# Optimization experiments

Hardware: AMD Instinct MI355X
Metric: run time of the kernel (lower is better)

## Reference

```python
import jax, jax.numpy as jnp
from jax import lax
import numpy as np

SIGMA = 0.4        # guided-attention diagonal width
PAD_MAG = 1e12     # -inf surrogate used by the torch viterbi


def _viterbi_align(logp, text_lens, mel_lens):
    """Monotonic forced alignment. logp: (B, L, T). Returns hard alignment (B, L, T)."""
    B, L, T = logp.shape
    neg = jnp.asarray(-PAD_MAG, logp.dtype)
    # ---- forward DP over time (lax.scan replaces the python loop over T) ----
    init = jnp.full((B, L), neg, logp.dtype).at[:, 0].set(logp[:, 0, 0])
    lp_T = jnp.moveaxis(logp, 2, 0)  # (T, B, L)

    def fwd(prev, lp_t):
        # transition: stay at same text token, or advance by one (shift down along L)
        shifted = jnp.concatenate([jnp.full((B, 1), neg, logp.dtype), prev[:, :-1]], axis=1)
        cur = jnp.maximum(prev, shifted) + lp_t
        return cur, cur

    _, betas = lax.scan(fwd, init, lp_T[1:])
    log_beta = jnp.concatenate([init[None], betas], axis=0)  # (T, B, L), indexed [t, b, l]

    # ---- backtracking (faithful to the float row/col arithmetic in the source) ----
    barange = jnp.arange(B)
    rows0 = (text_lens - 1).astype(logp.dtype)
    cols0 = (mel_lens - 1).astype(logp.dtype)

    def bwd(carry, _):
        rows, cols = carry
        r = rows.astype(jnp.int32)
        c = cols.astype(jnp.int32)
        cm1 = (c - 1) % T  # torch negative indexing wraps; emulate with mod
        g_go = log_beta[cm1, barange, (r - 1) % L]
        g_stay = log_beta[cm1, barange, r % L]
        is_go = (g_go > g_stay).astype(logp.dtype)
        new_rows = jnp.maximum(rows - is_go + 1.0, 0.0) - 1.0  # relu(x)-1 as in source
        new_cols = jnp.maximum(cols, 0.0) - 1.0
        return (new_rows, new_cols), new_rows

    _, rows_seq = lax.scan(bwd, (rows0, cols0), None, length=T - 1)  # r_1 .. r_{T-1}
    path = jnp.concatenate([rows_seq[::-1], rows0[None]], axis=0).T  # (B, T)

    # one-hot over text positions (static width L instead of path.max()+1)
    align = (path[:, :, None] == jnp.arange(L, dtype=path.dtype)[None, None, :]).astype(logp.dtype)  # (B,T,L)

    # per-batch shift: drop first (T - mel_len) frames, zero-pad at the end
    pad = T - mel_lens  # (B,)
    t_idx = jnp.arange(T)[None, :] + pad[:, None]  # (B, T)
    valid = (t_idx < T)
    gathered = jnp.take_along_axis(align, jnp.clip(t_idx, 0, T - 1)[:, :, None], axis=1)
    align = gathered * valid[:, :, None].astype(logp.dtype)
    return jnp.swapaxes(align, 1, 2)  # (B, L, T)


def _guided_attention_loss(att_ws, ilens, olens, sigma=SIGMA):
    """att_ws: (B, T_out, T_in). Masked guided-attention loss (scalar)."""
    B, T, L = att_ws.shape
    t = jnp.arange(T, dtype=att_ws.dtype)[None, :, None]
    l = jnp.arange(L, dtype=att_ws.dtype)[None, None, :]
    il = ilens.astype(att_ws.dtype)[:, None, None]
    ol = olens.astype(att_ws.dtype)[:, None, None]
    w = 1.0 - jnp.exp(-((l / il - t / ol) ** 2) / (2.0 * sigma * sigma))
    valid = (t < ol) & (l < il)
    return jnp.sum(jnp.where(valid, w * att_ws, 0.0)) / jnp.sum(olens).astype(att_ws.dtype)


def setup_inputs() -> dict:
    key = jax.random.key(0)
    k1, k2, k3, k4 = jax.random.split(key, 4)
    B, L, T = 32, 256, 2048
    log_prob_matrix = jax.nn.log_softmax(jax.random.normal(k1, (B, L, T), jnp.float32), axis=1)
    att_ws = jax.nn.softmax(jax.random.normal(k2, (B, T, L), jnp.float32), axis=-1)
    text_lengths = jax.random.randint(k3, (B,), L // 2, L + 1, dtype=jnp.int32)
    mel_lengths = jax.random.randint(k4, (B,), T // 2, T + 1, dtype=jnp.int32)
    return {
        "log_prob_matrix": log_prob_matrix,
        "att_ws": att_ws,
        "text_lengths": text_lengths,
        "mel_lengths": mel_lengths,
    }


def reference(log_prob_matrix, att_ws, text_lengths, mel_lengths):
    # n_frames_per_step = 1 -> olens = mel_lengths (clamped to att width T, trivially true)
    loss = _guided_attention_loss(att_ws, text_lengths, mel_lengths)
    align = _viterbi_align(log_prob_matrix, text_lengths, mel_lengths)
    return loss, align
```

## Files before the change

### kernel.cpp

```cpp
#include <hip/hip_runtime.h>
#include <cstdint>

#define NEG (-1e12f)
constexpr int Bn = 32, Ln = 256, Tn = 2048;
constexpr int TB = Tn / 64;


__device__ inline float dpp_ror1(float x) {
    int xi = __float_as_int(x);
    return __int_as_float(__builtin_amdgcn_update_dpp(xi, xi, 0x13C, 0xF, 0xF, false));
}

__device__ inline uint32_t lds_off(const void* p) {
    return (uint32_t)(uintptr_t)(__attribute__((address_space(3))) const void*)p;
}

#define BARRIER() { asm volatile("" ::: "memory"); \
                    __builtin_amdgcn_s_barrier(); \
                    asm volatile("" ::: "memory"); }

#define DSRX(DST, ROW, BUF) \
    asm volatile("ds_read_b128 %0, %1 offset:%c2" \
        : "=&v"(DST) \
        : "v"((((ROW) >> 2) & 1) ? vxb : vxa), \
          "i"((BUF) * 16384 + ((ROW) & 15) * 1024));

#define W4 { asm volatile("s_waitcnt lgkmcnt(4)"); __builtin_amdgcn_sched_barrier(0); }

#define ABIT(ACC, X, Y) \
    asm("v_cmp_gt_f32 vcc, %1, %2\n\tv_addc_co_u32 %0, vcc, %0, %0, vcc" \
        : "+v"(ACC) : "v"(X), "v"(Y) : "vcc");

#define STEPS(S, Q) { \
    if ((((S) - 1) & 32) == 0) { ABIT(a0hi, svp, pv0) } else { ABIT(a0lo, svp, pv0) } \
    float c3 = fmaxf(pv3, pv2) + (Q).w; \
    float sv = dpp_ror1(c3); \
    float c2 = fmaxf(pv2, pv1) + (Q).z; \
    float c1 = fmaxf(pv1, pv0) + (Q).y; \
    float lf = isl0 ? negc : svp; \
    float c0 = fmaxf(pv0, lf) + (Q).x; \
    if (((S) & 32) == 0) { \
        ABIT(a1hi, c0, c1) ABIT(a2hi, c1, c2) ABIT(a3hi, c2, c3) \
    } else { \
        ABIT(a1lo, c0, c1) ABIT(a2lo, c1, c2) ABIT(a3lo, c2, c3) \
    } \
    if ((S) == 63) { \
        bb[(size_t)(4 * lane + 1) * TB + m] = ((uint64_t)a1hi << 32) | a1lo; \
        bb[(size_t)(4 * lane + 2) * TB + m] = ((uint64_t)a2hi << 32) | a2lo; \
        bb[(size_t)(4 * lane + 3) * TB + m] = ((uint64_t)a3hi << 32) | a3lo; \
        a1lo = a1hi = a2lo = a2hi = a3lo = a3hi = 0; \
    } \
    if ((S) == 64) { \
        bb[(size_t)(4 * lane + 0) * TB + m] = ((uint64_t)a0hi << 32) | a0lo; \
        a0lo = a0hi = 0; \
    } \
    pv0 = c0; pv1 = c1; pv2 = c2; pv3 = c3; svp = sv; }

#define COMP16X(I) { \
    W4 \
    STEPS(16*(I)+ 1, qq0) STEPS(16*(I)+ 2, qq1) STEPS(16*(I)+ 3, qq2) STEPS(16*(I)+ 4, qq3) \
    DSRX(qq0,  9, (I)) DSRX(qq1, 10, (I)) DSRX(qq2, 11, (I)) DSRX(qq3, 12, (I)) \
    W4 \
    STEPS(16*(I)+ 5, qq4) STEPS(16*(I)+ 6, qq5) STEPS(16*(I)+ 7, qq6) STEPS(16*(I)+ 8, qq7) \
    DSRX(qq4, 13, (I)) DSRX(qq5, 14, (I)) DSRX(qq6, 15, (I)) DSRX(qq7,  0, ((I)+1)&3) \
    W4 \
    STEPS(16*(I)+ 9, qq0) STEPS(16*(I)+10, qq1) STEPS(16*(I)+11, qq2) STEPS(16*(I)+12, qq3) \
    DSRX(qq0,  1, ((I)+1)&3) DSRX(qq1,  2, ((I)+1)&3) DSRX(qq2,  3, ((I)+1)&3) DSRX(qq3,  4, ((I)+1)&3) \
    W4 \
    STEPS(16*(I)+13, qq4) STEPS(16*(I)+14, qq5) STEPS(16*(I)+15, qq6) STEPS(16*(I)+16, qq7) \
    DSRX(qq4,  5, ((I)+1)&3) DSRX(qq5,  6, ((I)+1)&3) DSRX(qq6,  7, ((I)+1)&3) DSRX(qq7,  8, ((I)+1)&3) \
    BARRIER() }

#define PLOAD(P) { \
    xh0 = *(const float4*)(pr0 + 16 * (P)); \
    xh1 = *(const float4*)(pr1 + 16 * (P)); \
    xh2 = *(const float4*)(pr2 + 16 * (P)); \
    xh3 = *(const float4*)(pr3 + 16 * (P)); \
    xh4 = *(const float4*)(pr4 + 16 * (P)); \
    if (six) xh5 = *(const float4*)(pr5 + 16 * (P)); }

#define PW1(XH, CC) { float* rq = rr + (CC); \
    rq[0] = (XH).x; rq[256] = (XH).y; rq[512] = (XH).z; rq[768] = (XH).w; }

#define PWRITE(P) { \
    float* rr = smem + ((P) & 3) * 4096; \
    PW1(xh0, c0) PW1(xh1, c1) PW1(xh2, c2) PW1(xh3, c3) PW1(xh4, c4) \
    if (six) PW1(xh5, c5) }

__global__ void __launch_bounds__(256, 1) k_mega(
        const float* __restrict__ logp, const float* __restrict__ att,
        const int* __restrict__ ilen, const int* __restrict__ olen,
        uint64_t* __restrict__ bits, float* __restrict__ partial,
        float* __restrict__ out) {
    __shared__ __align__(16) float smem[24576];
    int bid = blockIdx.x, tid = threadIdx.x;

    if (bid < 32) {
        int b = bid;
        if (tid < 64) {
            __builtin_amdgcn_s_setprio(1);
            int lane = tid;
            bool isl0 = (lane == 0);
            uint64_t* bb = bits + (size_t)b * (Ln * TB);
            const float negc = NEG;
            uint32_t lb = lds_off(smem) + (uint32_t)(lane * 16);
            uint32_t vxa = lb, vxb = lb ^ 64;

            float pv0, pv1, pv2, pv3, svp;
            uint32_t a0lo = 0, a0hi = 0, a1lo = 0, a1hi = 0;
            uint32_t a2lo = 0, a2hi = 0, a3lo = 0, a3hi = 0;

            {
                float lp00 = logp[(size_t)b * (Ln * Tn)];
                pv0 = isl0 ? lp00 : NEG;
                pv1 = NEG; pv2 = NEG; pv3 = NEG;
                svp = dpp_ror1(pv3);
                a1hi = (pv0 > pv1) ? 1u : 0u;
                a2hi = (pv1 > pv2) ? 1u : 0u;
                a3hi = (pv2 > pv3) ? 1u : 0u;
            }

            BARRIER();
            float4 qq0, qq1, qq2, qq3, qq4, qq5, qq6, qq7;
            DSRX(qq0, 1, 0) DSRX(qq1, 2, 0) DSRX(qq2, 3, 0) DSRX(qq3, 4, 0)
            DSRX(qq4, 5, 0) DSRX(qq5, 6, 0) DSRX(qq6, 7, 0) DSRX(qq7, 8, 0)

            for (int m = 0; m < 32; ++m) {
                COMP16X(0) COMP16X(1) COMP16X(2) COMP16X(3)
            }
            asm volatile("s_waitcnt vmcnt(0)" ::: "memory");
        } else {
            int tid2 = tid - 64;
            bool six = (tid2 < 64);
            const float* lpb = logp + (size_t)b * (Ln * Tn);
            int v0 = tid2, v1 = tid2 + 192, v2 = tid2 + 384,
                v3 = tid2 + 576, v4 = tid2 + 768, v5 = tid2 + 960;
            const float* pr0 = lpb + (size_t)(v0 >> 2) * Tn + 4 * (v0 & 3);
            const float* pr1 = lpb + (size_t)(v1 >> 2) * Tn + 4 * (v1 & 3);
            const float* pr2 = lpb + (size_t)(v2 >> 2) * Tn + 4 * (v2 & 3);
            const float* pr3 = lpb + (size_t)(v3 >> 2) * Tn + 4 * (v3 & 3);
            const float* pr4 = lpb + (size_t)(v4 >> 2) * Tn + 4 * (v4 & 3);
            const float* pr5 = lpb + (size_t)(v5 >> 2) * Tn + 4 * (v5 & 3);
            int c0 = (4 * (v0 & 3)) * 256 + ((v0 >> 2) ^ ((v0 & 1) << 4));
            int c1 = (4 * (v1 & 3)) * 256 + ((v1 >> 2) ^ ((v1 & 1) << 4));
            int c2 = (4 * (v2 & 3)) * 256 + ((v2 >> 2) ^ ((v2 & 1) << 4));
            int c3 = (4 * (v3 & 3)) * 256 + ((v3 >> 2) ^ ((v3 & 1) << 4));
            int c4 = (4 * (v4 & 3)) * 256 + ((v4 >> 2) ^ ((v4 & 1) << 4));
            int c5 = (4 * (v5 & 3)) * 256 + ((v5 >> 2) ^ ((v5 & 1) << 4));
            float4 xh0, xh1, xh2, xh3, xh4, xh5;

            PLOAD(0) PWRITE(0)
            PLOAD(1) PWRITE(1)
            PLOAD(2)
            asm volatile("s_waitcnt lgkmcnt(0)" ::: "memory");
            BARRIER();

            for (int k = 0; k < 128; ++k) {
                if (k <= 125) PWRITE(k + 2)
                if (k <= 124) PLOAD(k + 3)
                asm volatile("s_waitcnt lgkmcnt(0)" ::: "memory");
                BARRIER();
            }
        }
    } else if (bid < 32 + 1024) {
        const int N4 = Bn * Tn * Ln / 4;
        int j = bid - 32;
        int idx = j * 256 + tid;
        int stride = 1024 * 256;
        float acc = 0.f;
        for (int v = idx; v < N4; v += stride) {
            int flat = v << 2;
            int b  = flat >> 19;
            int t  = (flat >> 8) & (Tn - 1);
            int l0 = flat & (Ln - 1);
            int ili = ilen[b];
            int oli = olen[b];
            if (t >= oli) continue;
            float il = (float)ili, ol = (float)oli;
            float tf = (float)t / ol;
            float4 a = reinterpret_cast<const float4*>(att)[v];
            #pragma unroll
            for (int c = 0; c < 4; ++c) {
                int l = l0 + c;
                float av = (c == 0) ? a.x : (c == 1) ? a.y : (c == 2) ? a.z : a.w;
                if (l < ili) {
                    float d = (float)l / il - tf;
                    acc += (1.f - __expf(-d * d * 3.125f)) * av;
                }
            }
        }
        for (int off = 32; off > 0; off >>= 1) acc += __shfl_down(acc, off, 64);
        float* sw = smem;
        if ((tid & 63) == 0) sw[tid >> 6] = acc;
        __syncthreads();
        if (tid == 0) partial[j] = (sw[0] + sw[1]) + (sw[2] + sw[3]);
    } else {
        const int NZ = (Bn * Ln * Tn) / 4;
        int j = bid - 1056;
        float4 z = make_float4(0.f, 0.f, 0.f, 0.f);
        for (int i = j * 256 + tid; i < NZ; i += 1024 * 256)
            reinterpret_cast<float4*>(out)[i] = z;
        if (j == 0 && tid == 0) out[(size_t)Bn * Ln * Tn] = 0.f;
    }
}

__global__ void __launch_bounds__(256) k_tail(const uint64_t* __restrict__ bits,
                                              const int* __restrict__ ilen,
                                              const int* __restrict__ olen,
                                              const float* __restrict__ partial,
                                              float* __restrict__ out) {
    __shared__ uint64_t sb[Ln * TB];
    __shared__ int2 eb[Ln];
    __shared__ float sw[4];
    int b = blockIdx.x, tid = threadIdx.x;
    eb[tid] = make_int2(1, 0);
    const ulonglong2* g = (const ulonglong2*)(bits + (size_t)b * (Ln * TB));
    ulonglong2* s2 = (ulonglong2*)sb;
    #pragma unroll
    for (int i = 0; i < 16; ++i) s2[i * 256 + tid] = g[i * 256 + tid];
    __syncthreads();

    if (tid == 0) {
        int tl = ilen[b], ml = olen[b];
        int r = tl - 1, hi = ml - 1, p = ml - 2;
        if (p < 0) { eb[r] = make_int2(0, hi); }
        else {
            int c = p >> 6;
            #define LDW(RR) __builtin_bitreverse64(sb[(RR) * TB + c])
            uint64_t w0 = LDW(r);
            uint64_t w1 = LDW(r > 0 ? r - 1 : 0);
            uint64_t w2 = LDW(r > 1 ? r - 2 : 0);
            uint64_t w3 = LDW(r > 2 ? r - 3 : 0);
            int vd = 3;
            while (true) {
                int pb = p & 63;
                uint64_t mask = (pb == 63) ? ~0ull : ((1ull << (pb + 1)) - 1ull);
                uint64_t mm = w0 & mask;
                if (mm == 0) {
                    p = (p & ~63) - 1;
                    if (p < 0) { eb[r] = make_int2(0, hi); break; }
                    c = p >> 6;
                    w0 = LDW(r);
                    w1 = LDW(r > 0 ? r - 1 : 0);
                    w2 = LDW(r > 1 ? r - 2 : 0);
                    w3 = LDW(r > 2 ? r - 3 : 0);
                    vd = 3;
                } else {
                    int q = 63 - __builtin_clzll(mm);
                    int tq = (p & ~63) + q;
                    eb[r] = make_int2(tq + 1, hi);
                    r -= 1;
                    if (r < 0) break;
                    hi = tq;
                    p = tq - 1;
                    if (p < 0) { eb[r] = make_int2(0, hi); break; }
                    w0 = w1; w1 = w2; w2 = w3; vd -= 1;
                    int nc = p >> 6;
                    if (nc != c || vd == 0) {
                        c = nc;
                        w0 = LDW(r);
                        w1 = LDW(r > 0 ? r - 1 : 0);
                        w2 = LDW(r > 1 ? r - 2 : 0);
                        w3 = LDW(r > 2 ? r - 3 : 0);
                        vd = 3;
                    }
                }
            }
            #undef LDW
        }
    }
    __syncthreads();

    {
        int2 e = eb[tid];
        float* orow = out + 1 + (((size_t)b * Ln + tid) << 11);
        for (int t = e.x; t <= e.y; ++t) orow[t] = 1.f;
    }

    if (b == 0) {
        float acc = 0.f;
        for (int i = tid; i < 1024; i += 256) acc += partial[i];
        for (int off = 32; off > 0; off >>= 1) acc += __shfl_down(acc, off, 64);
        if ((tid & 63) == 0) sw[tid >> 6] = acc;
        __syncthreads();
        if (tid == 0) {
            float tot = (sw[0] + sw[1]) + (sw[2] + sw[3]);
            int so = 0;
            for (int i = 0; i < Bn; ++i) so += olen[i];
            out[0] = tot / (float)so;
        }
    }
}

extern "C" void kernel_launch(void* const* d_in, const int* in_sizes, int n_in,
                              void* d_out, int out_size, void* d_ws, size_t ws_size,
                              hipStream_t stream) {
    const float* logp = (const float*)d_in[0];
    const float* att  = (const float*)d_in[1];
    const int* tlen   = (const int*)d_in[2];
    const int* mlen   = (const int*)d_in[3];
    float* out = (float*)d_out;
    uint64_t* bits = (uint64_t*)d_ws;
    float* partial = (float*)((char*)d_ws + 2097152);

    k_mega<<<32 + 1024 + 1024, 256, 0, stream>>>(logp, att, tlen, mlen,
                                                 bits, partial, out);
    k_tail<<<Bn, 256, 0, stream>>>(bits, tlen, mlen, partial, out);
}
```

Measured before the change: 130.4 us.

## Throttle zero-fill blocks with fewer, sleeping workers and deepen backtrack word prefetch

```diff
diff --git a/kernel.cpp b/kernel.cpp
--- a/kernel.cpp
+++ b/kernel.cpp
@@ -198,8 +198,10 @@
         const int NZ = (Bn * Ln * Tn) / 4;
         int j = bid - 1056;
         float4 z = make_float4(0.f, 0.f, 0.f, 0.f);
-        for (int i = j * 256 + tid; i < NZ; i += 1024 * 256)
+        for (int i = j * 256 + tid; i < NZ; i += 224 * 256) {
             reinterpret_cast<float4*>(out)[i] = z;
+            asm volatile("s_sleep 48");
+        }
         if (j == 0 && tid == 0) out[(size_t)Bn * Ln * Tn] = 0.f;
     }
 }
@@ -225,13 +227,20 @@
         int r = tl - 1, hi = ml - 1, p = ml - 2;
         if (p < 0) { eb[r] = make_int2(0, hi); }
         else {
-            int c = p >> 6;
+            int c = p >> 6, vd;
+            uint64_t w0, w1, w2, w3, w4, w5, w6, w7;
             #define LDW(RR) __builtin_bitreverse64(sb[(RR) * TB + c])
-            uint64_t w0 = LDW(r);
-            uint64_t w1 = LDW(r > 0 ? r - 1 : 0);
-            uint64_t w2 = LDW(r > 1 ? r - 2 : 0);
-            uint64_t w3 = LDW(r > 2 ? r - 3 : 0);
-            int vd = 3;
+            #define RELOAD() { \
+                w0 = LDW(r); \
+                w1 = LDW(r > 0 ? r - 1 : 0); \
+                w2 = LDW(r > 1 ? r - 2 : 0); \
+                w3 = LDW(r > 2 ? r - 3 : 0); \
+                w4 = LDW(r > 3 ? r - 4 : 0); \
+                w5 = LDW(r > 4 ? r - 5 : 0); \
+                w6 = LDW(r > 5 ? r - 6 : 0); \
+                w7 = LDW(r > 6 ? r - 7 : 0); \
+                vd = 7; }
+            RELOAD();
             while (true) {
                 int pb = p & 63;
                 uint64_t mask = (pb == 63) ? ~0ull : ((1ull << (pb + 1)) - 1ull);
@@ -240,11 +249,7 @@
                     p = (p & ~63) - 1;
                     if (p < 0) { eb[r] = make_int2(0, hi); break; }
                     c = p >> 6;
-                    w0 = LDW(r);
-                    w1 = LDW(r > 0 ? r - 1 : 0);
-                    w2 = LDW(r > 1 ? r - 2 : 0);
-                    w3 = LDW(r > 2 ? r - 3 : 0);
-                    vd = 3;
+                    RELOAD();
                 } else {
                     int q = 63 - __builtin_clzll(mm);
                     int tq = (p & ~63) + q;
@@ -254,18 +259,13 @@
                     hi = tq;
                     p = tq - 1;
                     if (p < 0) { eb[r] = make_int2(0, hi); break; }
-                    w0 = w1; w1 = w2; w2 = w3; vd -= 1;
+                    w0 = w1; w1 = w2; w2 = w3; w3 = w4; w4 = w5; w5 = w6; w6 = w7;
+                    vd -= 1;
                     int nc = p >> 6;
-                    if (nc != c || vd == 0) {
-                        c = nc;
-                        w0 = LDW(r);
-                        w1 = LDW(r > 0 ? r - 1 : 0);
-                        w2 = LDW(r > 1 ? r - 2 : 0);
-                        w3 = LDW(r > 2 ? r - 3 : 0);
-                        vd = 3;
-                    }
+                    if (nc != c || vd == 0) { c = nc; RELOAD(); }
                 }
             }
+            #undef RELOAD
             #undef LDW
         }
     }
@@ -303,7 +303,7 @@
     uint64_t* bits = (uint64_t*)d_ws;
     float* partial = (float*)((char*)d_ws + 2097152);
 
-    k_mega<<<32 + 1024 + 1024, 256, 0, stream>>>(logp, att, tlen, mlen,
-                                                 bits, partial, out);
+    k_mega<<<32 + 1024 + 224, 256, 0, stream>>>(logp, att, tlen, mlen,
+                                                bits, partial, out);
     k_tail<<<Bn, 256, 0, stream>>>(bits, tlen, mlen, partial, out);
 }
```

New measurement: 185.5 us. 1.42x slower.
